# Performance work log

Measured on AMD Instinct MI355X. Metric: run time of the kernel, lower is better.

Reference implementation:

```python
import jax, jax.numpy as jnp
import numpy as np

G, V_PER, E_PER = 512, 400, 800
N, E = G * V_PER, G * E_PER
NF, H, F, OUT = 128, 64, 8, 64  # n_features, filtration_hidden, n_filtrations, out_dim


def _p(k, shape, fan_in):
    return jax.random.normal(k, shape, jnp.float32) * (1.0 / np.sqrt(fan_in))


def setup_inputs() -> dict:
    key = jax.random.key(0)
    ks = jax.random.split(key, 24)
    x = jax.random.normal(ks[0], (N, NF), jnp.float32)
    pos = jax.random.normal(ks[1], (N, 3), jnp.float32)
    # per-graph random edges, no self loops (dedup'ed single-direction edge list)
    src_l = jax.random.randint(ks[2], (E,), 0, V_PER)
    off = jax.random.randint(ks[3], (E,), 1, V_PER)
    dst_l = (src_l + off) % V_PER
    g = jnp.arange(E, dtype=jnp.int32) // E_PER
    edge_index = jnp.stack([g * V_PER + src_l, g * V_PER + dst_l]).astype(jnp.int32)
    vertex_slices = (jnp.arange(G + 1, dtype=jnp.int32) * V_PER)
    edge_slices = (jnp.arange(G + 1, dtype=jnp.int32) * E_PER)
    batch = jnp.repeat(jnp.arange(G, dtype=jnp.int32), V_PER)
    return {
        'x': x, 'pos': pos, 'edge_index': edge_index,
        'vertex_slices': vertex_slices, 'edge_slices': edge_slices, 'batch': batch,
        'W1': _p(ks[4], (NF, H), NF), 'b1': jnp.zeros((H,), jnp.float32),
        'W2': _p(ks[5], (H, F), H), 'b2': jnp.zeros((F,), jnp.float32),
        'We1': _p(ks[6], (NF + 1, H), NF + 1), 'be1': jnp.zeros((H,), jnp.float32),
        'We2': _p(ks[7], (H, F), H), 'be2': jnp.zeros((F,), jnp.float32),
        'Wd0': _p(ks[8], (F * 4, OUT), F * 4), 'bd0': jnp.zeros((OUT,), jnp.float32),
        'Wd1': _p(ks[9], (4, OUT), 4), 'bd1': jnp.zeros((OUT,), jnp.float32),
        'bn_gamma': jnp.ones((OUT,), jnp.float32), 'bn_beta': jnp.zeros((OUT,), jnp.float32),
        'Wo1': _p(ks[10], (OUT, OUT), OUT), 'bo1': jnp.zeros((OUT,), jnp.float32),
        'Wo2': _p(ks[11], (OUT, OUT), OUT), 'bo2': jnp.zeros((OUT,), jnp.float32),
    }


def reference(x, pos, edge_index, vertex_slices, edge_slices, batch,
              W1, b1, W2, b2, We1, be1, We2, be2,
              Wd0, bd0, Wd1, bd1, bn_gamma, bn_beta, Wo1, bo1, Wo2, bo2):
    n_graphs = vertex_slices.shape[0] - 1
    src, dst = edge_index[0], edge_index[1]
    mlp = lambda h, Wa, ba, Wb, bb: jax.nn.sigmoid(jnp.maximum(h @ Wa + ba, 0.0) @ Wb + bb)
    # vertex filtrations [N, F]
    fv = mlp(x, W1, b1, W2, b2)
    # edge filtrations: gather endpoint features + euclidean distance, small MLP [E, F]
    dist = jnp.sqrt(jnp.sum((pos[src] - pos[dst]) ** 2, axis=-1))
    fe = mlp(jnp.concatenate([x[src] + x[dst], dist[:, None]], axis=-1), We1, be1, We2, be2)
    # dim-0 rephine tuples (vectorizable surrogate for the CPU union-find pairing):
    # per vertex, death = min incident edge filtration, gamma = max incident edge
    # filtration; isolated vertices -> 1.0 (mirrors the NaN -> 1.0 fixup).
    dmin = jnp.full((x.shape[0], fe.shape[1]), jnp.inf, fe.dtype).at[src].min(fe).at[dst].min(fe)
    dmin = jnp.where(jnp.isinf(dmin), 1.0, dmin)
    dmax = jnp.full((x.shape[0], fe.shape[1]), -jnp.inf, fe.dtype).at[src].max(fe).at[dst].max(fe)
    dmax = jnp.where(jnp.isinf(dmax), 1.0, dmax)
    # raw (b, d, g) -> reorder [0, 2, 1] -> prepend 0  =>  (0, b, g, d), shape [N, F, 4]
    pers0 = jnp.stack([jnp.zeros_like(fv), fv, dmax, dmin], axis=-1)
    # DeepSetLayer0: Linear then scatter-mean over graphs -> [G, OUT]
    lin0 = pers0.reshape(x.shape[0], -1) @ Wd0 + bd0
    cnt_v = jax.ops.segment_sum(jnp.ones((x.shape[0],), lin0.dtype), batch, num_segments=n_graphs)
    x0 = jax.ops.segment_sum(lin0, batch, num_segments=n_graphs) / cnt_v[:, None]
    # dim-1: cycle edges = edges beyond the spanning-tree count per graph. After the
    # original's nonzero -> 1.0 assignment the dim-1 tuples are binary (0,1,1,1).
    eidx = jnp.arange(src.shape[0], dtype=jnp.int32)
    batch_e = jnp.searchsorted(edge_slices, eidx, side='right').astype(jnp.int32) - 1
    e_local = eidx - edge_slices[batch_e]
    nv = vertex_slices[batch_e + 1] - vertex_slices[batch_e]
    cyc = (e_local >= nv - 1).astype(lin0.dtype)  # [E]
    row = cyc[:, None] * jnp.array([0.0, 1.0, 1.0, 1.0], lin0.dtype)
    lin1 = row @ Wd1 + bd1  # [E, OUT]
    num = jax.ops.segment_sum(cyc[:, None] * lin1, batch_e, num_segments=n_graphs)
    den = jax.ops.segment_sum(cyc, batch_e, num_segments=n_graphs)
    x1 = jnp.where(den[:, None] > 0, num / jnp.maximum(den, 1.0)[:, None], 0.0)
    # identical across the F filtrations (binary tuples), so mean over F == x1
    h = x0 + x1
    # BatchNorm1d (training-mode batch stats, fresh affine params)
    mu = h.mean(axis=0)
    var = jnp.mean((h - mu) ** 2, axis=0)
    h = (h - mu) / jnp.sqrt(var + 1e-5) * bn_gamma + bn_beta
    # out MLP
    return jnp.maximum(h @ Wo1 + bo1, 0.0) @ Wo2 + bo2
```

## Files before the change

kernel.cpp:

```cpp
#include <hip/hip_runtime.h>
#include <math.h>

#define NV 204800
#define NE 409600
#define NG 512
#define V_PER 400
#define E_PER 800

#define BM 128
#define KT 32

__device__ __forceinline__ int wswz(int j) { return j ^ (((j >> 5) & 1) << 2); }

__global__ __launch_bounds__(256)
void k_proj(const float* __restrict__ x, const float* __restrict__ W1,
            const float* __restrict__ b1, const float* __restrict__ W2,
            const float* __restrict__ b2, const float* __restrict__ We1,
            float* __restrict__ fv, float* __restrict__ y2) {
  __shared__ __align__(16) char smem[33280];
  float (*xt)[BM] = (float (*)[BM])smem;
  float (*Wt)[BM] = (float (*)[BM])(smem + KT * BM * 4);
  float (*hs)[65] = (float (*)[65])smem;
  __shared__ float W2s[64 * 8];

  const int tid = threadIdx.x;
  const long vb = (long)blockIdx.x * BM;

  if (tid < 128) ((float4*)W2s)[tid] = ((const float4*)W2)[tid];

  const int v = tid >> 1, h = tid & 1;
  const int jg = tid & 15, rg = tid >> 4;

  const int wb0 = wswz(jg * 8);
  const int wb1 = wswz(jg * 8 + 4);

  float acc[8][8];
  #pragma unroll
  for (int i = 0; i < 8; ++i)
    #pragma unroll
    for (int j = 0; j < 8; ++j) acc[i][j] = 0.f;

  #pragma unroll 1
  for (int t = 0; t < 4; ++t) {
    {
      const float4* src = (const float4*)(x + (vb + v) * 128 + t * KT + h * 16);
      const float4 a0 = src[0], a1 = src[1], a2 = src[2], a3 = src[3];
      const int r = h * 16;
      xt[r + 0][v] = a0.x; xt[r + 1][v] = a0.y; xt[r + 2][v] = a0.z; xt[r + 3][v] = a0.w;
      xt[r + 4][v] = a1.x; xt[r + 5][v] = a1.y; xt[r + 6][v] = a1.z; xt[r + 7][v] = a1.w;
      xt[r + 8][v] = a2.x; xt[r + 9][v] = a2.y; xt[r +10][v] = a2.z; xt[r +11][v] = a2.w;
      xt[r +12][v] = a3.x; xt[r +13][v] = a3.y; xt[r +14][v] = a3.z; xt[r +15][v] = a3.w;
      #pragma unroll
      for (int q = 0; q < 2; ++q) {
        const int idx = tid + q * 256;
        const int kk = idx >> 4, j4 = idx & 15;
        const float4 wa = ((const float4*)(W1 + t * KT * 64))[idx];
        const float4 wb = ((const float4*)(We1 + t * KT * 64))[idx];
        *(float4*)&Wt[kk][wswz(j4 * 4)] = wa;
        *(float4*)&Wt[kk][wswz(64 + j4 * 4)] = wb;
      }
    }
    __syncthreads();
    #pragma unroll
    for (int kk = 0; kk < KT; ++kk) {
      const float4 av0 = *(const float4*)&xt[kk][rg * 8];
      const float4 av1 = *(const float4*)&xt[kk][rg * 8 + 4];
      const float4 w0 = *(const float4*)&Wt[kk][wb0];
      const float4 w1 = *(const float4*)&Wt[kk][wb1];
      const float a[8] = {av0.x, av0.y, av0.z, av0.w, av1.x, av1.y, av1.z, av1.w};
      const float w[8] = {w0.x, w0.y, w0.z, w0.w, w1.x, w1.y, w1.z, w1.w};
      #pragma unroll
      for (int i = 0; i < 8; ++i)
        #pragma unroll
        for (int j = 0; j < 8; ++j) acc[i][j] = fmaf(a[i], w[j], acc[i][j]);
    }
    __syncthreads();
  }

  if (jg < 8) {
    const float4 b1a = *(const float4*)(b1 + jg * 8);
    const float4 b1b = *(const float4*)(b1 + jg * 8 + 4);
    #pragma unroll
    for (int i = 0; i < 8; ++i) {
      const int row = rg * 8 + i;
      *(float4*)&hs[row][jg * 8] = make_float4(
          fmaxf(acc[i][0] + b1a.x, 0.f), fmaxf(acc[i][1] + b1a.y, 0.f),
          fmaxf(acc[i][2] + b1a.z, 0.f), fmaxf(acc[i][3] + b1a.w, 0.f));
      *(float4*)&hs[row][jg * 8 + 4] = make_float4(
          fmaxf(acc[i][4] + b1b.x, 0.f), fmaxf(acc[i][5] + b1b.y, 0.f),
          fmaxf(acc[i][6] + b1b.z, 0.f), fmaxf(acc[i][7] + b1b.w, 0.f));
    }
  } else {
    #pragma unroll
    for (int i = 0; i < 8; ++i) {
      const long row = vb + rg * 8 + i;
      *(float4*)&y2[row * 64 + (jg - 8) * 8] =
          make_float4(acc[i][0], acc[i][1], acc[i][2], acc[i][3]);
      *(float4*)&y2[row * 64 + (jg - 8) * 8 + 4] =
          make_float4(acc[i][4], acc[i][5], acc[i][6], acc[i][7]);
    }
  }
  __syncthreads();

  const int jg2 = tid & 7, eg2 = tid >> 3;
  float p[4][8];
  #pragma unroll
  for (int i = 0; i < 4; ++i)
    #pragma unroll
    for (int o = 0; o < 8; ++o) p[i][o] = 0.f;
  #pragma unroll
  for (int jj = 0; jj < 8; ++jj) {
    const float4 w20 = *(const float4*)&W2s[(jg2 * 8 + jj) * 8];
    const float4 w21 = *(const float4*)&W2s[(jg2 * 8 + jj) * 8 + 4];
    const float w2r[8] = {w20.x, w20.y, w20.z, w20.w, w21.x, w21.y, w21.z, w21.w};
    #pragma unroll
    for (int i = 0; i < 4; ++i) {
      const float hv = hs[eg2 * 4 + i][jg2 * 8 + jj];
      #pragma unroll
      for (int o = 0; o < 8; ++o) p[i][o] = fmaf(hv, w2r[o], p[i][o]);
    }
  }
  #pragma unroll
  for (int m = 1; m <= 4; m <<= 1)
    #pragma unroll
    for (int i = 0; i < 4; ++i)
      #pragma unroll
      for (int o = 0; o < 8; ++o) p[i][o] += __shfl_xor(p[i][o], m, 64);

  if (jg2 < 4) {
    const float4 b2a = *(const float4*)b2;
    const float4 b2b = *(const float4*)(b2 + 4);
    const float b2r[8] = {b2a.x, b2a.y, b2a.z, b2a.w, b2b.x, b2b.y, b2b.z, b2b.w};
    const long row = vb + eg2 * 4 + jg2;
    float vout[8];
    #pragma unroll
    for (int o = 0; o < 8; ++o) vout[o] = 1.0f / (1.0f + __expf(-(p[jg2][o] + b2r[o])));
    *(float4*)&fv[row * 8]     = make_float4(vout[0], vout[1], vout[2], vout[3]);
    *(float4*)&fv[row * 8 + 4] = make_float4(vout[4], vout[5], vout[6], vout[7]);
  }
}

__global__ __launch_bounds__(256)
void k_edge_finish(const float* __restrict__ y2, const float* __restrict__ pos,
                   const int* __restrict__ srcp, const int* __restrict__ dstp,
                   const float* __restrict__ We1, const float* __restrict__ be1,
                   const float* __restrict__ We2, const float* __restrict__ be2,
                   float* __restrict__ fe) {
  const int tid = threadIdx.x;
  const int jg = tid & 7;
  const long ebase = (long)blockIdx.x * 256;

  float w2[64];
  #pragma unroll
  for (int q = 0; q < 16; ++q)
    *(float4*)&w2[q * 4] = ((const float4*)(We2 + jg * 64))[q];
  const float4 wda = *(const float4*)(We1 + 128 * 64 + jg * 8);
  const float4 wdb = *(const float4*)(We1 + 128 * 64 + jg * 8 + 4);
  const float4 bea = *(const float4*)(be1 + jg * 8);
  const float4 beb = *(const float4*)(be1 + jg * 8 + 4);
  const float wd[8] = {wda.x, wda.y, wda.z, wda.w, wdb.x, wdb.y, wdb.z, wdb.w};
  const float be[8] = {bea.x, bea.y, bea.z, bea.w, beb.x, beb.y, beb.z, beb.w};
  const float4 b2a = *(const float4*)be2;
  const float4 b2b = *(const float4*)(be2 + 4);

  #pragma unroll 1
  for (int ps = 0; ps < 8; ++ps) {
    const long e = ebase + ps * 32 + (tid >> 3);
    const int s = srcp[e], d = dstp[e];
    const float4 a0 = *(const float4*)(y2 + (long)s * 64 + jg * 8);
    const float4 a1 = *(const float4*)(y2 + (long)s * 64 + jg * 8 + 4);
    const float4 c0 = *(const float4*)(y2 + (long)d * 64 + jg * 8);
    const float4 c1 = *(const float4*)(y2 + (long)d * 64 + jg * 8 + 4);
    const float dx = pos[s * 3 + 0] - pos[d * 3 + 0];
    const float dy = pos[s * 3 + 1] - pos[d * 3 + 1];
    const float dz = pos[s * 3 + 2] - pos[d * 3 + 2];
    const float dist = sqrtf(dx * dx + dy * dy + dz * dz);
    float hh[8] = {a0.x + c0.x, a0.y + c0.y, a0.z + c0.z, a0.w + c0.w,
                   a1.x + c1.x, a1.y + c1.y, a1.z + c1.z, a1.w + c1.w};
    float p[8];
    #pragma unroll
    for (int o = 0; o < 8; ++o) p[o] = 0.f;
    #pragma unroll
    for (int jj = 0; jj < 8; ++jj) {
      const float hv = fmaxf(fmaf(dist, wd[jj], hh[jj] + be[jj]), 0.f);
      #pragma unroll
      for (int o = 0; o < 8; ++o) p[o] = fmaf(hv, w2[jj * 8 + o], p[o]);
    }
    #pragma unroll
    for (int m = 1; m <= 4; m <<= 1)
      #pragma unroll
      for (int o = 0; o < 8; ++o) p[o] += __shfl_xor(p[o], m, 64);
    if (jg == 0) {
      float vout[8];
      const float b2r[8] = {b2a.x, b2a.y, b2a.z, b2a.w, b2b.x, b2b.y, b2b.z, b2b.w};
      #pragma unroll
      for (int o = 0; o < 8; ++o) vout[o] = 1.0f / (1.0f + __expf(-(p[o] + b2r[o])));
      *(float4*)&fe[e * 8]     = make_float4(vout[0], vout[1], vout[2], vout[3]);
      *(float4*)&fe[e * 8 + 4] = make_float4(vout[4], vout[5], vout[6], vout[7]);
    }
  }
}

__global__ __launch_bounds__(256, 2)
void k_graph_reduce(const float* __restrict__ fv, const float* __restrict__ fe,
                    const int* __restrict__ srcp, const int* __restrict__ dstp,
                    const float* __restrict__ Wd0, const float* __restrict__ bd0,
                    const float* __restrict__ Wd1, const float* __restrict__ bd1,
                    float* __restrict__ hbuf) {
  __shared__ unsigned dminS[8 * V_PER];
  __shared__ unsigned dmaxS[8 * V_PER];
  __shared__ float red[256];
  __shared__ float sums[3][8];
  const int tid = threadIdx.x;
  const int g = blockIdx.x;

  for (int i = tid; i < 8 * V_PER; i += 256) {
    dminS[i] = 0x7F800000u;
    dmaxS[i] = 0u;
  }
  __syncthreads();

  const int eb = g * E_PER;
  const int vb = g * V_PER;
  for (int e = tid; e < E_PER; e += 256) {
    const int ls = srcp[eb + e] - vb;
    const int ld = dstp[eb + e] - vb;
    const uint4 f0 = ((const uint4*)(fe + (long)(eb + e) * 8))[0];
    const uint4 f1 = ((const uint4*)(fe + (long)(eb + e) * 8))[1];
    const unsigned fb[8] = {f0.x, f0.y, f0.z, f0.w, f1.x, f1.y, f1.z, f1.w};
    #pragma unroll
    for (int f = 0; f < 8; ++f) {
      atomicMin(&dminS[f * V_PER + ls], fb[f]);
      atomicMax(&dmaxS[f * V_PER + ls], fb[f]);
      atomicMin(&dminS[f * V_PER + ld], fb[f]);
      atomicMax(&dmaxS[f * V_PER + ld], fb[f]);
    }
  }
  __syncthreads();

  const int f = tid & 7;
  float sfv = 0.f, smin = 0.f, smax = 0.f;
  for (int v = tid >> 3; v < V_PER; v += 32) {
    sfv += fv[(long)(vb + v) * 8 + f];
    const unsigned mn = dminS[f * V_PER + v];
    if (mn == 0x7F800000u) { smin += 1.0f; smax += 1.0f; }
    else { smin += __uint_as_float(mn); smax += __uint_as_float(dmaxS[f * V_PER + v]); }
  }
  red[tid] = sfv; __syncthreads();
  for (int s = 128; s >= 8; s >>= 1) { if (tid < s) red[tid] += red[tid + s]; __syncthreads(); }
  if (tid < 8) sums[0][tid] = red[tid];
  __syncthreads();
  red[tid] = smax; __syncthreads();
  for (int s = 128; s >= 8; s >>= 1) { if (tid < s) red[tid] += red[tid + s]; __syncthreads(); }
  if (tid < 8) sums[1][tid] = red[tid];
  __syncthreads();
  red[tid] = smin; __syncthreads();
  for (int s = 128; s >= 8; s >>= 1) { if (tid < s) red[tid] += red[tid + s]; __syncthreads(); }
  if (tid < 8) sums[2][tid] = red[tid];
  __syncthreads();

  if (tid < 64) {
    const int o = tid;
    const float inv = 1.0f / (float)V_PER;
    float acc = bd0[o];
    #pragma unroll
    for (int ff = 0; ff < 8; ++ff) {
      acc = fmaf(sums[0][ff] * inv, Wd0[(4 * ff + 1) * 64 + o], acc);
      acc = fmaf(sums[1][ff] * inv, Wd0[(4 * ff + 2) * 64 + o], acc);
      acc = fmaf(sums[2][ff] * inv, Wd0[(4 * ff + 3) * 64 + o], acc);
    }
    const float x1 = Wd1[64 + o] + Wd1[128 + o] + Wd1[192 + o] + bd1[o];
    hbuf[g * 64 + o] = acc + x1;
  }
}

__global__ __launch_bounds__(256)
void k_bn_stats(const float* __restrict__ hbuf, float* __restrict__ mu,
                float* __restrict__ rstd) {
  __shared__ float rs[256], rs2[256];
  const int tid = threadIdx.x;
  const int c = tid & 63, rg = tid >> 6;
  float s = 0.f, s2 = 0.f;
  for (int r = rg * 128; r < rg * 128 + 128; ++r) {
    const float v = hbuf[r * 64 + c];
    s += v; s2 += v * v;
  }
  rs[tid] = s; rs2[tid] = s2; __syncthreads();
  if (tid < 128) { rs[tid] += rs[tid + 128]; rs2[tid] += rs2[tid + 128]; }
  __syncthreads();
  if (tid < 64) {
    const float st = rs[tid] + rs[tid + 64];
    const float st2 = rs2[tid] + rs2[tid + 64];
    const float m = st / 512.0f;
    const float var = st2 / 512.0f - m * m;
    mu[tid] = m;
    rstd[tid] = rsqrtf(var + 1e-5f);
  }
}

__global__ __launch_bounds__(256)
void k_out_mlp(const float* __restrict__ hbuf, const float* __restrict__ mu,
               const float* __restrict__ rstd, const float* __restrict__ gam,
               const float* __restrict__ bet, const float* __restrict__ Wo1,
               const float* __restrict__ bo1, const float* __restrict__ Wo2,
               const float* __restrict__ bo2, float* __restrict__ out) {
  __shared__ float W1s[64 * 64], W2s[64 * 64];
  __shared__ float hn[4][64], t1[4][64];
  __shared__ float mus[64], rstds[64], gs[64], bs[64], b1s[64], b2s[64];
  const int tid = threadIdx.x;
  for (int i = tid; i < 4096; i += 256) { W1s[i] = Wo1[i]; W2s[i] = Wo2[i]; }
  if (tid < 64) {
    mus[tid] = mu[tid]; rstds[tid] = rstd[tid]; gs[tid] = gam[tid];
    bs[tid] = bet[tid]; b1s[tid] = bo1[tid]; b2s[tid] = bo2[tid];
  }
  __syncthreads();
  const int r = tid >> 6, o = tid & 63;
  for (int it = 0; it < 4; ++it) {
    const int row = blockIdx.x * 16 + it * 4 + r;
    hn[r][o] = (hbuf[row * 64 + o] - mus[o]) * rstds[o] * gs[o] + bs[o];
    __syncthreads();
    float a = b1s[o];
    #pragma unroll 8
    for (int i = 0; i < 64; ++i) a = fmaf(hn[r][i], W1s[i * 64 + o], a);
    t1[r][o] = fmaxf(a, 0.f);
    __syncthreads();
    float a2 = b2s[o];
    #pragma unroll 8
    for (int i = 0; i < 64; ++i) a2 = fmaf(t1[r][i], W2s[i * 64 + o], a2);
    out[row * 64 + o] = a2;
    __syncthreads();
  }
}

extern "C" void kernel_launch(void* const* d_in, const int* in_sizes, int n_in,
                              void* d_out, int out_size, void* d_ws, size_t ws_size,
                              hipStream_t stream) {
  const float* x   = (const float*)d_in[0];
  const float* pos = (const float*)d_in[1];
  const int*   ei  = (const int*)d_in[2];
  const float* W1  = (const float*)d_in[6];
  const float* b1  = (const float*)d_in[7];
  const float* W2  = (const float*)d_in[8];
  const float* b2  = (const float*)d_in[9];
  const float* We1 = (const float*)d_in[10];
  const float* be1 = (const float*)d_in[11];
  const float* We2 = (const float*)d_in[12];
  const float* be2 = (const float*)d_in[13];
  const float* Wd0 = (const float*)d_in[14];
  const float* bd0 = (const float*)d_in[15];
  const float* Wd1 = (const float*)d_in[16];
  const float* bd1 = (const float*)d_in[17];
  const float* gam = (const float*)d_in[18];
  const float* bet = (const float*)d_in[19];
  const float* Wo1 = (const float*)d_in[20];
  const float* bo1 = (const float*)d_in[21];
  const float* Wo2 = (const float*)d_in[22];
  const float* bo2 = (const float*)d_in[23];

  const int* srcp = ei;
  const int* dstp = ei + NE;

  float* fv   = (float*)d_ws;
  float* fe   = fv + (size_t)NV * 8;
  float* hb   = fe + (size_t)NE * 8;
  float* mu   = hb + NG * 64;
  float* rstd = mu + 64;
  float* y2   = rstd + 64;

  hipLaunchKernelGGL(k_proj, dim3(NV / BM), dim3(256), 0, stream,
                     x, W1, b1, W2, b2, We1, fv, y2);
  hipLaunchKernelGGL(k_edge_finish, dim3(NE / 256), dim3(256), 0, stream,
                     y2, pos, srcp, dstp, We1, be1, We2, be2, fe);
  hipLaunchKernelGGL(k_graph_reduce, dim3(NG), dim3(256), 0, stream,
                     fv, fe, srcp, dstp, Wd0, bd0, Wd1, bd1, hb);
  hipLaunchKernelGGL(k_bn_stats, dim3(1), dim3(256), 0, stream, hb, mu, rstd);
  hipLaunchKernelGGL(k_out_mlp, dim3(NG / 16), dim3(256), 0, stream,
                     hb, mu, rstd, gam, bet, Wo1, bo1, Wo2, bo2, (float*)d_out);
}
```

Measured before the change: 370.3 us.

## Fuse edge MLP into per-graph reduce, double-buffer projection tiles, fold BN stats

Merges the edge filtration MLP into the per-graph reduction kernel, so edge sigmoid values go straight into shared-memory min/max atomics and the fe buffer never round-trips through global memory. The projection GEMM now double-buffers its x/W shared tiles with register prefetch, overlapping global loads with FMAs. BatchNorm statistics are accumulated with global atomics in the reduce kernel, which removes the single-block stats kernel. In exchange the fused kernel runs only 512 blocks each holding 800 edges, which may lower parallelism for the gather. The doubled shared memory in k_proj may also cut its occupancy.

Result: slower. 684.7 us (+84.9%).

```diff
diff --git a/kernel.cpp b/kernel.cpp
--- a/kernel.cpp
+++ b/kernel.cpp
@@ -17,9 +17,7 @@
             const float* __restrict__ b1, const float* __restrict__ W2,
             const float* __restrict__ b2, const float* __restrict__ We1,
             float* __restrict__ fv, float* __restrict__ y2) {
-  __shared__ __align__(16) char smem[33280];
-  float (*xt)[BM] = (float (*)[BM])smem;
-  float (*Wt)[BM] = (float (*)[BM])(smem + KT * BM * 4);
+  __shared__ __align__(16) char smem[66560];
   float (*hs)[65] = (float (*)[65])smem;
   __shared__ float W2s[64 * 8];
 
@@ -30,37 +28,52 @@
 
   const int v = tid >> 1, h = tid & 1;
   const int jg = tid & 15, rg = tid >> 4;
-
   const int wb0 = wswz(jg * 8);
   const int wb1 = wswz(jg * 8 + 4);
 
+  float4 px[4], pw[4];
+
+  auto load_regs = [&](int t) {
+    const float4* src = (const float4*)(x + (vb + v) * 128 + t * KT + h * 16);
+    px[0] = src[0]; px[1] = src[1]; px[2] = src[2]; px[3] = src[3];
+    pw[0] = ((const float4*)(W1 + t * KT * 64))[tid];
+    pw[1] = ((const float4*)(W1 + t * KT * 64))[tid + 256];
+    pw[2] = ((const float4*)(We1 + t * KT * 64))[tid];
+    pw[3] = ((const float4*)(We1 + t * KT * 64))[tid + 256];
+  };
+  auto store_tile = [&](int b) {
+    float (*xt)[BM] = (float (*)[BM])(smem + b * 32768);
+    float (*Wt)[BM] = (float (*)[BM])(smem + b * 32768 + 16384);
+    const int r = h * 16;
+    xt[r + 0][v] = px[0].x; xt[r + 1][v] = px[0].y; xt[r + 2][v] = px[0].z; xt[r + 3][v] = px[0].w;
+    xt[r + 4][v] = px[1].x; xt[r + 5][v] = px[1].y; xt[r + 6][v] = px[1].z; xt[r + 7][v] = px[1].w;
+    xt[r + 8][v] = px[2].x; xt[r + 9][v] = px[2].y; xt[r +10][v] = px[2].z; xt[r +11][v] = px[2].w;
+    xt[r +12][v] = px[3].x; xt[r +13][v] = px[3].y; xt[r +14][v] = px[3].z; xt[r +15][v] = px[3].w;
+    #pragma unroll
+    for (int q = 0; q < 2; ++q) {
+      const int idx = tid + q * 256;
+      const int kk = idx >> 4, j4 = idx & 15;
+      *(float4*)&Wt[kk][wswz(j4 * 4)] = pw[q];
+      *(float4*)&Wt[kk][wswz(64 + j4 * 4)] = pw[2 + q];
+    }
+  };
+
   float acc[8][8];
   #pragma unroll
   for (int i = 0; i < 8; ++i)
     #pragma unroll
     for (int j = 0; j < 8; ++j) acc[i][j] = 0.f;
+
+  load_regs(0);
+  store_tile(0);
+  __syncthreads();
 
   #pragma unroll 1
   for (int t = 0; t < 4; ++t) {
-    {
-      const float4* src = (const float4*)(x + (vb + v) * 128 + t * KT + h * 16);
-      const float4 a0 = src[0], a1 = src[1], a2 = src[2], a3 = src[3];
-      const int r = h * 16;
-      xt[r + 0][v] = a0.x; xt[r + 1][v] = a0.y; xt[r + 2][v] = a0.z; xt[r + 3][v] = a0.w;
-      xt[r + 4][v] = a1.x; xt[r + 5][v] = a1.y; xt[r + 6][v] = a1.z; xt[r + 7][v] = a1.w;
-      xt[r + 8][v] = a2.x; xt[r + 9][v] = a2.y; xt[r +10][v] = a2.z; xt[r +11][v] = a2.w;
-      xt[r +12][v] = a3.x; xt[r +13][v] = a3.y; xt[r +14][v] = a3.z; xt[r +15][v] = a3.w;
-      #pragma unroll
-      for (int q = 0; q < 2; ++q) {
-        const int idx = tid + q * 256;
-        const int kk = idx >> 4, j4 = idx & 15;
-        const float4 wa = ((const float4*)(W1 + t * KT * 64))[idx];
-        const float4 wb = ((const float4*)(We1 + t * KT * 64))[idx];
-        *(float4*)&Wt[kk][wswz(j4 * 4)] = wa;
-        *(float4*)&Wt[kk][wswz(64 + j4 * 4)] = wb;
-      }
-    }
-    __syncthreads();
+    if (t < 3) load_regs(t + 1);
+    const int b = t & 1;
+    float (*xt)[BM] = (float (*)[BM])(smem + b * 32768);
+    float (*Wt)[BM] = (float (*)[BM])(smem + b * 32768 + 16384);
     #pragma unroll
     for (int kk = 0; kk < KT; ++kk) {
       const float4 av0 = *(const float4*)&xt[kk][rg * 8];
@@ -74,6 +87,7 @@
         #pragma unroll
         for (int j = 0; j < 8; ++j) acc[i][j] = fmaf(a[i], w[j], acc[i][j]);
     }
+    if (t < 3) store_tile((t + 1) & 1);
     __syncthreads();
   }
 
@@ -141,14 +155,26 @@
 }
 
 __global__ __launch_bounds__(256)
-void k_edge_finish(const float* __restrict__ y2, const float* __restrict__ pos,
-                   const int* __restrict__ srcp, const int* __restrict__ dstp,
-                   const float* __restrict__ We1, const float* __restrict__ be1,
-                   const float* __restrict__ We2, const float* __restrict__ be2,
-                   float* __restrict__ fe) {
+void k_reduce(const float* __restrict__ fv, const float* __restrict__ y2,
+              const float* __restrict__ pos,
+              const int* __restrict__ srcp, const int* __restrict__ dstp,
+              const float* __restrict__ We1, const float* __restrict__ be1,
+              const float* __restrict__ We2, const float* __restrict__ be2,
+              const float* __restrict__ Wd0, const float* __restrict__ bd0,
+              const float* __restrict__ Wd1, const float* __restrict__ bd1,
+              float* __restrict__ hbuf, float* __restrict__ bnacc) {
+  __shared__ unsigned dminS[8 * V_PER];
+  __shared__ unsigned dmaxS[8 * V_PER];
+  __shared__ float red[256];
+  __shared__ float sums[3][8];
   const int tid = threadIdx.x;
-  const int jg = tid & 7;
-  const long ebase = (long)blockIdx.x * 256;
+  const int g = blockIdx.x;
+  const int jg = tid & 7, eslot = tid >> 3;
+
+  for (int i = tid; i < 8 * V_PER; i += 256) {
+    dminS[i] = 0x7F800000u;
+    dmaxS[i] = 0u;
+  }
 
   float w2[64];
   #pragma unroll
@@ -160,12 +186,15 @@
   const float4 beb = *(const float4*)(be1 + jg * 8 + 4);
   const float wd[8] = {wda.x, wda.y, wda.z, wda.w, wdb.x, wdb.y, wdb.z, wdb.w};
   const float be[8] = {bea.x, bea.y, bea.z, bea.w, beb.x, beb.y, beb.z, beb.w};
-  const float4 b2a = *(const float4*)be2;
-  const float4 b2b = *(const float4*)(be2 + 4);
-
-  #pragma unroll 1
-  for (int ps = 0; ps < 8; ++ps) {
-    const long e = ebase + ps * 32 + (tid >> 3);
+  const float be2o = be2[jg];
+  __syncthreads();
+
+  const int eb = g * E_PER;
+  const int vb = g * V_PER;
+
+  #pragma unroll 2
+  for (int pass = 0; pass < E_PER / 32; ++pass) {
+    const long e = eb + pass * 32 + eslot;
     const int s = srcp[e], d = dstp[e];
     const float4 a0 = *(const float4*)(y2 + (long)s * 64 + jg * 8);
     const float4 a1 = *(const float4*)(y2 + (long)s * 64 + jg * 8 + 4);
@@ -175,8 +204,8 @@
     const float dy = pos[s * 3 + 1] - pos[d * 3 + 1];
     const float dz = pos[s * 3 + 2] - pos[d * 3 + 2];
     const float dist = sqrtf(dx * dx + dy * dy + dz * dz);
-    float hh[8] = {a0.x + c0.x, a0.y + c0.y, a0.z + c0.z, a0.w + c0.w,
-                   a1.x + c1.x, a1.y + c1.y, a1.z + c1.z, a1.w + c1.w};
+    const float hh[8] = {a0.x + c0.x, a0.y + c0.y, a0.z + c0.z, a0.w + c0.w,
+                         a1.x + c1.x, a1.y + c1.y, a1.z + c1.z, a1.w + c1.w};
     float p[8];
     #pragma unroll
     for (int o = 0; o < 8; ++o) p[o] = 0.f;
@@ -190,61 +219,26 @@
     for (int m = 1; m <= 4; m <<= 1)
       #pragma unroll
       for (int o = 0; o < 8; ++o) p[o] += __shfl_xor(p[o], m, 64);
-    if (jg == 0) {
-      float vout[8];
-      const float b2r[8] = {b2a.x, b2a.y, b2a.z, b2a.w, b2b.x, b2b.y, b2b.z, b2b.w};
-      #pragma unroll
-      for (int o = 0; o < 8; ++o) vout[o] = 1.0f / (1.0f + __expf(-(p[o] + b2r[o])));
-      *(float4*)&fe[e * 8]     = make_float4(vout[0], vout[1], vout[2], vout[3]);
-      *(float4*)&fe[e * 8 + 4] = make_float4(vout[4], vout[5], vout[6], vout[7]);
-    }
-  }
-}
-
-__global__ __launch_bounds__(256, 2)
-void k_graph_reduce(const float* __restrict__ fv, const float* __restrict__ fe,
-                    const int* __restrict__ srcp, const int* __restrict__ dstp,
-                    const float* __restrict__ Wd0, const float* __restrict__ bd0,
-                    const float* __restrict__ Wd1, const float* __restrict__ bd1,
-                    float* __restrict__ hbuf) {
-  __shared__ unsigned dminS[8 * V_PER];
-  __shared__ unsigned dmaxS[8 * V_PER];
-  __shared__ float red[256];
-  __shared__ float sums[3][8];
-  const int tid = threadIdx.x;
-  const int g = blockIdx.x;
-
-  for (int i = tid; i < 8 * V_PER; i += 256) {
-    dminS[i] = 0x7F800000u;
-    dmaxS[i] = 0u;
-  }
-  __syncthreads();
-
-  const int eb = g * E_PER;
-  const int vb = g * V_PER;
-  for (int e = tid; e < E_PER; e += 256) {
-    const int ls = srcp[eb + e] - vb;
-    const int ld = dstp[eb + e] - vb;
-    const uint4 f0 = ((const uint4*)(fe + (long)(eb + e) * 8))[0];
-    const uint4 f1 = ((const uint4*)(fe + (long)(eb + e) * 8))[1];
-    const unsigned fb[8] = {f0.x, f0.y, f0.z, f0.w, f1.x, f1.y, f1.z, f1.w};
-    #pragma unroll
-    for (int f = 0; f < 8; ++f) {
-      atomicMin(&dminS[f * V_PER + ls], fb[f]);
-      atomicMax(&dmaxS[f * V_PER + ls], fb[f]);
-      atomicMin(&dminS[f * V_PER + ld], fb[f]);
-      atomicMax(&dmaxS[f * V_PER + ld], fb[f]);
-    }
+    float pf = p[0];
+    #pragma unroll
+    for (int o = 1; o < 8; ++o) pf = (jg == o) ? p[o] : pf;
+    const float fev = 1.0f / (1.0f + __expf(-(pf + be2o)));
+    const unsigned bits = __float_as_uint(fev);
+    const int ls = s - vb, ld = d - vb;
+    atomicMin(&dminS[jg * V_PER + ls], bits);
+    atomicMax(&dmaxS[jg * V_PER + ls], bits);
+    atomicMin(&dminS[jg * V_PER + ld], bits);
+    atomicMax(&dmaxS[jg * V_PER + ld], bits);
   }
   __syncthreads();
 
   const int f = tid & 7;
   float sfv = 0.f, smin = 0.f, smax = 0.f;
-  for (int v = tid >> 3; v < V_PER; v += 32) {
-    sfv += fv[(long)(vb + v) * 8 + f];
-    const unsigned mn = dminS[f * V_PER + v];
+  for (int vv = tid >> 3; vv < V_PER; vv += 32) {
+    sfv += fv[(long)(vb + vv) * 8 + f];
+    const unsigned mn = dminS[f * V_PER + vv];
     if (mn == 0x7F800000u) { smin += 1.0f; smax += 1.0f; }
-    else { smin += __uint_as_float(mn); smax += __uint_as_float(dmaxS[f * V_PER + v]); }
+    else { smin += __uint_as_float(mn); smax += __uint_as_float(dmaxS[f * V_PER + vv]); }
   }
   red[tid] = sfv; __syncthreads();
   for (int s = 128; s >= 8; s >>= 1) { if (tid < s) red[tid] += red[tid + s]; __syncthreads(); }
@@ -270,48 +264,31 @@
       acc = fmaf(sums[2][ff] * inv, Wd0[(4 * ff + 3) * 64 + o], acc);
     }
     const float x1 = Wd1[64 + o] + Wd1[128 + o] + Wd1[192 + o] + bd1[o];
-    hbuf[g * 64 + o] = acc + x1;
+    const float hv = acc + x1;
+    hbuf[g * 64 + o] = hv;
+    atomicAdd(&bnacc[o], hv);
+    atomicAdd(&bnacc[64 + o], hv * hv);
   }
 }
 
 __global__ __launch_bounds__(256)
-void k_bn_stats(const float* __restrict__ hbuf, float* __restrict__ mu,
-                float* __restrict__ rstd) {
-  __shared__ float rs[256], rs2[256];
-  const int tid = threadIdx.x;
-  const int c = tid & 63, rg = tid >> 6;
-  float s = 0.f, s2 = 0.f;
-  for (int r = rg * 128; r < rg * 128 + 128; ++r) {
-    const float v = hbuf[r * 64 + c];
-    s += v; s2 += v * v;
-  }
-  rs[tid] = s; rs2[tid] = s2; __syncthreads();
-  if (tid < 128) { rs[tid] += rs[tid + 128]; rs2[tid] += rs2[tid + 128]; }
-  __syncthreads();
-  if (tid < 64) {
-    const float st = rs[tid] + rs[tid + 64];
-    const float st2 = rs2[tid] + rs2[tid + 64];
-    const float m = st / 512.0f;
-    const float var = st2 / 512.0f - m * m;
-    mu[tid] = m;
-    rstd[tid] = rsqrtf(var + 1e-5f);
-  }
-}
-
-__global__ __launch_bounds__(256)
-void k_out_mlp(const float* __restrict__ hbuf, const float* __restrict__ mu,
-               const float* __restrict__ rstd, const float* __restrict__ gam,
-               const float* __restrict__ bet, const float* __restrict__ Wo1,
-               const float* __restrict__ bo1, const float* __restrict__ Wo2,
-               const float* __restrict__ bo2, float* __restrict__ out) {
+void k_out_mlp(const float* __restrict__ hbuf, const float* __restrict__ bnacc,
+               const float* __restrict__ gam, const float* __restrict__ bet,
+               const float* __restrict__ Wo1, const float* __restrict__ bo1,
+               const float* __restrict__ Wo2, const float* __restrict__ bo2,
+               float* __restrict__ out) {
   __shared__ float W1s[64 * 64], W2s[64 * 64];
   __shared__ float hn[4][64], t1[4][64];
   __shared__ float mus[64], rstds[64], gs[64], bs[64], b1s[64], b2s[64];
   const int tid = threadIdx.x;
   for (int i = tid; i < 4096; i += 256) { W1s[i] = Wo1[i]; W2s[i] = Wo2[i]; }
   if (tid < 64) {
-    mus[tid] = mu[tid]; rstds[tid] = rstd[tid]; gs[tid] = gam[tid];
-    bs[tid] = bet[tid]; b1s[tid] = bo1[tid]; b2s[tid] = bo2[tid];
+    const float s = bnacc[tid], s2 = bnacc[64 + tid];
+    const float m = s * (1.0f / 512.0f);
+    const float var = s2 * (1.0f / 512.0f) - m * m;
+    mus[tid] = m; rstds[tid] = rsqrtf(var + 1e-5f);
+    gs[tid] = gam[tid]; bs[tid] = bet[tid];
+    b1s[tid] = bo1[tid]; b2s[tid] = bo2[tid];
   }
   __syncthreads();
   const int r = tid >> 6, o = tid & 63;
@@ -360,20 +337,17 @@
   const int* srcp = ei;
   const int* dstp = ei + NE;
 
-  float* fv   = (float*)d_ws;
-  float* fe   = fv + (size_t)NV * 8;
-  float* hb   = fe + (size_t)NE * 8;
-  float* mu   = hb + NG * 64;
-  float* rstd = mu + 64;
-  float* y2   = rstd + 64;
-
+  float* fv    = (float*)d_ws;
+  float* hb    = fv + (size_t)NV * 8;
+  float* bnacc = hb + (size_t)NG * 64;
+  float* y2    = bnacc + 128;
+
+  hipMemsetAsync(bnacc, 0, 128 * sizeof(float), stream);
   hipLaunchKernelGGL(k_proj, dim3(NV / BM), dim3(256), 0, stream,
                      x, W1, b1, W2, b2, We1, fv, y2);
-  hipLaunchKernelGGL(k_edge_finish, dim3(NE / 256), dim3(256), 0, stream,
-                     y2, pos, srcp, dstp, We1, be1, We2, be2, fe);
-  hipLaunchKernelGGL(k_graph_reduce, dim3(NG), dim3(256), 0, stream,
-                     fv, fe, srcp, dstp, Wd0, bd0, Wd1, bd1, hb);
-  hipLaunchKernelGGL(k_bn_stats, dim3(1), dim3(256), 0, stream, hb, mu, rstd);
+  hipLaunchKernelGGL(k_reduce, dim3(NG), dim3(256), 0, stream,
+                     fv, y2, pos, srcp, dstp, We1, be1, We2, be2,
+                     Wd0, bd0, Wd1, bd1, hb, bnacc);
   hipLaunchKernelGGL(k_out_mlp, dim3(NG / 16), dim3(256), 0, stream,
-                     hb, mu, rstd, gam, bet, Wo1, bo1, Wo2, bo2, (float*)d_out);
+                     hb, bnacc, gam, bet, Wo1, bo1, Wo2, bo2, (float*)d_out);
 }
```
